# Performance work log

Hardware: AMD Instinct MI355X
Metric: run time of the kernel (lower is better)

The kernel has to match this reference:

```python
import jax, jax.numpy as jnp
import numpy as np

DIM = 1024
HEADS = 16
DIM_HEAD = 64
INNER = HEADS * DIM_HEAD
EPS = 1e-5


def layernorm(x, g, b):
    mu = jnp.mean(x, axis=-1, keepdims=True)
    var = jnp.mean((x - mu) ** 2, axis=-1, keepdims=True)
    return (x - mu) * jax.lax.rsqrt(var + EPS) * g + b


def setup_inputs() -> dict:
    key = jax.random.key(0)
    ks = jax.random.split(key, 8)
    B, S = 2, 2048
    s_in = (2.0 / DIM) ** 0.5
    return {
        "x": jax.random.normal(ks[0], (B, S, DIM), jnp.float32),
        "w_qkv": jax.random.normal(ks[1], (DIM, 3 * INNER), jnp.float32) * s_in,
        "w_out": jax.random.normal(ks[2], (INNER, DIM), jnp.float32) * s_in,
        "b_out": jnp.zeros((DIM,), jnp.float32),
        "g1": jnp.ones((DIM,), jnp.float32),
        "beta1": jnp.zeros((DIM,), jnp.float32),
        "g2": jnp.ones((DIM,), jnp.float32),
        "beta2": jnp.zeros((DIM,), jnp.float32),
        "w_ff1": jax.random.normal(ks[3], (DIM, 4 * DIM), jnp.float32) * s_in,
        "b_ff1": jnp.zeros((4 * DIM,), jnp.float32),
        "w_ff2": jax.random.normal(ks[4], (4 * DIM, DIM), jnp.float32) * (2.0 / (4 * DIM)) ** 0.5,
        "b_ff2": jnp.zeros((DIM,), jnp.float32),
    }


def reference(x, w_qkv, w_out, b_out, g1, beta1, g2, beta2, w_ff1, b_ff1, w_ff2, b_ff2):
    B, S, D = x.shape
    scale = DIM_HEAD ** -0.5
    # --- attention block (pre-norm) ---
    h = layernorm(x, g1, beta1)
    qkv = h @ w_qkv  # [B,S,3*INNER]
    q, k, v = jnp.split(qkv, 3, axis=-1)
    def heads(t):
        return t.reshape(B, S, HEADS, DIM_HEAD).transpose(0, 2, 1, 3)  # [B,H,S,dh]
    q, k, v = heads(q), heads(k), heads(v)
    attn = jnp.einsum("bhsd,bhtd->bhst", q, k) * scale
    attn = jax.nn.softmax(attn, axis=-1)
    out = jnp.einsum("bhst,bhtd->bhsd", attn, v)
    out = out.transpose(0, 2, 1, 3).reshape(B, S, INNER)
    x = x + out @ w_out + b_out
    # --- FFN block (pre-norm) ---
    h = layernorm(x, g2, beta2)
    h = jax.nn.gelu(h @ w_ff1 + b_ff1, approximate=False)
    x = x + h @ w_ff2 + b_ff2
    return x
```

## Files before the change

### kernel.cpp

```cpp
#include <hip/hip_runtime.h>
#include <math.h>

typedef unsigned short u16;
typedef __attribute__((ext_vector_type(4))) float f32x4;
typedef __attribute__((ext_vector_type(16))) float f32x16;
typedef __attribute__((ext_vector_type(4))) unsigned short u16x4;
typedef __attribute__((ext_vector_type(8))) __bf16 bf16x8;

static constexpr int SS   = 2048;
static constexpr int DD   = 1024;
static constexpr int HH   = 16;
static constexpr int DH   = 64;
static constexpr int NTOK = 4096;
static constexpr int NQKV = 3072;

#define DEV static __device__ __forceinline__
#define GLD_AS1(p) ((__attribute__((address_space(1))) void*)(void*)(p))
#define GLD_AS3(p) ((__attribute__((address_space(3))) void*)(p))

#define WAIT_BAR(N) asm volatile("s_waitcnt vmcnt(" #N ")\n\ts_barrier" ::: "memory")
#define BAR()       asm volatile("s_barrier" ::: "memory")

DEV u16 f2bf(float f) {
    union { float f; unsigned int i; } v; v.f = f;
    unsigned int r = v.i + 0x7fffu + ((v.i >> 16) & 1u);
    return (u16)(r >> 16);
}
DEV float bdec(u16 u) {
    union { unsigned int i; float f; } v; v.i = ((unsigned int)u) << 16; return v.f;
}

DEV f32x4 MFMA(bf16x8 a, bf16x8 b, f32x4 c) {
    return __builtin_amdgcn_mfma_f32_16x16x32_bf16(a, b, c, 0, 0, 0);
}
DEV f32x16 MFMA32(bf16x8 a, bf16x8 b, f32x16 c) {
    return __builtin_amdgcn_mfma_f32_32x32x16_bf16(a, b, c, 0, 0, 0);
}
DEV f32x16 zero16() {
    f32x16 z;
    #pragma unroll
    for (int i = 0; i < 16; i++) z[i] = 0.f;
    return z;
}

__global__ __launch_bounds__(256)
void k_transpose(const float* __restrict__ in, u16* __restrict__ out, int R, int C) {
    __shared__ float tile[32][33];
    int c0 = blockIdx.x * 32, r0 = blockIdx.y * 32;
    int tx = threadIdx.x, ty = threadIdx.y;
    #pragma unroll
    for (int i = 0; i < 32; i += 8)
        tile[ty + i][tx] = in[(size_t)(r0 + ty + i) * C + c0 + tx];
    __syncthreads();
    #pragma unroll
    for (int i = 0; i < 32; i += 8)
        out[(size_t)(c0 + ty + i) * R + r0 + tx] = f2bf(tile[tx][ty + i]);
}

__global__ __launch_bounds__(256)
void k_transpose_v(const u16* __restrict__ qkv, u16* __restrict__ vT) {
    __shared__ u16 tile[32][33];
    int bid = blockIdx.x;
    int st = bid & 63;
    int dt = (bid >> 6) & 1;
    int bh = bid >> 7;
    int b = bh >> 4, h = bh & 15;
    int s0 = st * 32, d0 = dt * 32;
    int tx = threadIdx.x & 31, ty = threadIdx.x >> 5;
    const u16* src = qkv + ((size_t)(b * SS + s0)) * NQKV + 2048 + h * DH + d0;
    #pragma unroll
    for (int i = 0; i < 32; i += 8)
        tile[ty + i][tx] = src[(size_t)(ty + i) * NQKV + tx];
    __syncthreads();
    u16* dst = vT + ((size_t)bh * DH + d0) * SS + s0;
    #pragma unroll
    for (int i = 0; i < 32; i += 8)
        dst[(size_t)(ty + i) * SS + tx] = tile[tx][ty + i];
}

__global__ __launch_bounds__(256)
void k_layernorm(const float* __restrict__ x, const float* __restrict__ g,
                 const float* __restrict__ b, u16* __restrict__ out) {
    int row = blockIdx.x, t = threadIdx.x;
    const float4* xp = reinterpret_cast<const float4*>(x + (size_t)row * DD);
    float4 v = xp[t];
    float s = v.x + v.y + v.z + v.w;
    float q = v.x * v.x + v.y * v.y + v.z * v.z + v.w * v.w;
    #pragma unroll
    for (int m = 1; m < 64; m <<= 1) { s += __shfl_xor(s, m); q += __shfl_xor(q, m); }
    __shared__ float ps[4], pq[4];
    int w = t >> 6, l = t & 63;
    if (l == 0) { ps[w] = s; pq[w] = q; }
    __syncthreads();
    s = ps[0] + ps[1] + ps[2] + ps[3];
    q = pq[0] + pq[1] + pq[2] + pq[3];
    float mu = s * (1.0f / DD);
    float var = q * (1.0f / DD) - mu * mu;
    float rstd = rsqrtf(var + 1e-5f);
    float4 gv = reinterpret_cast<const float4*>(g)[t];
    float4 bv = reinterpret_cast<const float4*>(b)[t];
    u16x4 o;
    o.x = f2bf((v.x - mu) * rstd * gv.x + bv.x);
    o.y = f2bf((v.y - mu) * rstd * gv.y + bv.y);
    o.z = f2bf((v.z - mu) * rstd * gv.z + bv.z);
    o.w = f2bf((v.w - mu) * rstd * gv.w + bv.w);
    reinterpret_cast<u16x4*>(out + (size_t)row * DD)[t] = o;
}

__global__ __launch_bounds__(256)
void k_redln(const float* __restrict__ x, const u16* __restrict__ P0,
             const u16* __restrict__ P1, const float* __restrict__ bias,
             const float* __restrict__ g, const float* __restrict__ be,
             float* __restrict__ X1, u16* __restrict__ LNout) {
    int row = blockIdx.x, t = threadIdx.x;
    size_t i = (size_t)row * 256 + t;
    float4 xv = reinterpret_cast<const float4*>(x)[i];
    u16x4 a = reinterpret_cast<const u16x4*>(P0)[i];
    u16x4 bb = reinterpret_cast<const u16x4*>(P1)[i];
    float4 bv = reinterpret_cast<const float4*>(bias)[t];
    float4 v;
    v.x = xv.x + bdec(a.x) + bdec(bb.x) + bv.x;
    v.y = xv.y + bdec(a.y) + bdec(bb.y) + bv.y;
    v.z = xv.z + bdec(a.z) + bdec(bb.z) + bv.z;
    v.w = xv.w + bdec(a.w) + bdec(bb.w) + bv.w;
    reinterpret_cast<float4*>(X1)[i] = v;
    float s = v.x + v.y + v.z + v.w;
    float q = v.x * v.x + v.y * v.y + v.z * v.z + v.w * v.w;
    #pragma unroll
    for (int m = 1; m < 64; m <<= 1) { s += __shfl_xor(s, m); q += __shfl_xor(q, m); }
    __shared__ float ps[4], pq[4];
    int w = t >> 6, l = t & 63;
    if (l == 0) { ps[w] = s; pq[w] = q; }
    __syncthreads();
    s = ps[0] + ps[1] + ps[2] + ps[3];
    q = pq[0] + pq[1] + pq[2] + pq[3];
    float mu = s * (1.0f / DD);
    float var = q * (1.0f / DD) - mu * mu;
    float rstd = rsqrtf(var + 1e-5f);
    float4 gv = reinterpret_cast<const float4*>(g)[t];
    float4 ev = reinterpret_cast<const float4*>(be)[t];
    u16x4 o;
    o.x = f2bf((v.x - mu) * rstd * gv.x + ev.x);
    o.y = f2bf((v.y - mu) * rstd * gv.y + ev.y);
    o.z = f2bf((v.z - mu) * rstd * gv.z + ev.z);
    o.w = f2bf((v.w - mu) * rstd * gv.w + ev.w);
    reinterpret_cast<u16x4*>(LNout + (size_t)row * DD)[t] = o;
}

template<int MODE>
__global__ __launch_bounds__(256)
void k_gemm(const u16* __restrict__ A, const u16* __restrict__ BT,
            float* __restrict__ Cf, u16* __restrict__ Cb,
            const float* __restrict__ bias, const float* __restrict__ res,
            u16* __restrict__ vT, int M, int N, int K) {
    __shared__ __align__(128) char lds[2][32768];
    const int t = threadIdx.x;
    const int w = t >> 6, l = t & 63;
    const int lg = l >> 4, lr = l & 15;
    const int m0 = blockIdx.y * 128, n0 = blockIdx.x * 128;
    const int wr = w >> 1, wc = w & 1;

    int kbeg = 0, kend = K;
    if (MODE == 3) {
        const int kh = K >> 1;
        kbeg = blockIdx.z * kh;
        kend = kbeg + kh;
    }

    const int csw = ((l & 7) ^ (l >> 3)) << 3;
    const int chunk0 = w * 4;
    const int srow = (l >> 3);

    f32x4 acc[4][4];
    #pragma unroll
    for (int i = 0; i < 4; i++)
        #pragma unroll
        for (int j = 0; j < 4; j++)
            acc[i][j] = (f32x4){0.f, 0.f, 0.f, 0.f};

    #pragma unroll
    for (int i = 0; i < 4; i++) {
        const int chunk = chunk0 + i;
        const int r = chunk * 8 + srow;
        __builtin_amdgcn_global_load_lds(GLD_AS1(A  + (size_t)(m0 + r) * K + kbeg + csw),
                                         GLD_AS3(lds[0] + chunk * 1024), 16, 0, 0);
        __builtin_amdgcn_global_load_lds(GLD_AS1(BT + (size_t)(n0 + r) * K + kbeg + csw),
                                         GLD_AS3(lds[0] + 16384 + chunk * 1024), 16, 0, 0);
    }

    int buf = 0;
    for (int kt = kbeg; kt < kend; kt += 64) {
        if (kt + 64 < kend) {
            #pragma unroll
            for (int i = 0; i < 4; i++) {
                const int chunk = chunk0 + i;
                const int r = chunk * 8 + srow;
                __builtin_amdgcn_global_load_lds(GLD_AS1(A  + (size_t)(m0 + r) * K + kt + 64 + csw),
                                                 GLD_AS3(lds[buf ^ 1] + chunk * 1024), 16, 0, 0);
                __builtin_amdgcn_global_load_lds(GLD_AS1(BT + (size_t)(n0 + r) * K + kt + 64 + csw),
                                                 GLD_AS3(lds[buf ^ 1] + 16384 + chunk * 1024), 16, 0, 0);
            }
            WAIT_BAR(8);
        } else {
            WAIT_BAR(0);
        }
        const char* Al = lds[buf];
        const char* Bl = lds[buf] + 16384;
        #pragma unroll
        for (int s = 0; s < 2; s++) {
            const int swz = (s * 64 + lg * 16) ^ ((lr & 7) << 4);
            bf16x8 af[4], bfr[4];
            #pragma unroll
            for (int mi = 0; mi < 4; mi++)
                af[mi] = *reinterpret_cast<const bf16x8*>(Al + (wr * 64 + mi * 16 + lr) * 128 + swz);
            #pragma unroll
            for (int ni = 0; ni < 4; ni++)
                bfr[ni] = *reinterpret_cast<const bf16x8*>(Bl + (wc * 64 + ni * 16 + lr) * 128 + swz);
            #pragma unroll
            for (int mi = 0; mi < 4; mi++)
                #pragma unroll
                for (int ni = 0; ni < 4; ni++)
                    acc[mi][ni] = MFMA(af[mi], bfr[ni], acc[mi][ni]);
        }
        BAR();
        buf ^= 1;
    }

    #pragma unroll
    for (int mi = 0; mi < 4; mi++) {
        #pragma unroll
        for (int ni = 0; ni < 4; ni++) {
            int nn = n0 + wc * 64 + ni * 16 + lr;
            #pragma unroll
            for (int r = 0; r < 4; r++) {
                int mm = m0 + wr * 64 + mi * 16 + lg * 4 + r;
                float v = acc[mi][ni][r];
                if (MODE == 0) {
                    float sv = (nn < 1024) ? v * 0.18033688011112042f : v;
                    Cb[(size_t)mm * NQKV + nn] = f2bf(sv);
                } else if (MODE == 2) {
                    float u = v + bias[nn];
                    float u3 = u * u * u;
                    float gl = u / (1.0f + exp2f(-2.3022077f * u - 0.10294276f * u3));
                    Cb[(size_t)mm * N + nn] = f2bf(gl);
                } else {
                    u16* dst = blockIdx.z ? vT : Cb;
                    dst[(size_t)mm * N + nn] = f2bf(v);
                }
            }
        }
    }
}

__global__ __launch_bounds__(256)
void k_ffreduce(const float* __restrict__ RES, const u16* __restrict__ P0,
                const u16* __restrict__ P1, const float* __restrict__ bias,
                float* __restrict__ OUT) {
    int i = blockIdx.x * 256 + threadIdx.x;
    float4 xv = reinterpret_cast<const float4*>(RES)[i];
    u16x4 a = reinterpret_cast<const u16x4*>(P0)[i];
    u16x4 b = reinterpret_cast<const u16x4*>(P1)[i];
    float4 bv = reinterpret_cast<const float4*>(bias)[i & (DD / 4 - 1)];
    float4 o;
    o.x = xv.x + bdec(a.x) + bdec(b.x) + bv.x;
    o.y = xv.y + bdec(a.y) + bdec(b.y) + bv.y;
    o.z = xv.z + bdec(a.z) + bdec(b.z) + bv.z;
    o.w = xv.w + bdec(a.w) + bdec(b.w) + bv.w;
    reinterpret_cast<float4*>(OUT)[i] = o;
}

__global__ __launch_bounds__(256)
void k_attn(const u16* __restrict__ qkv, const u16* __restrict__ vT,
            u16* __restrict__ out) {
    const int w = threadIdx.x >> 6, l = threadIdx.x & 63;
    const int q = l & 31, hi = l >> 5;
    const int task = (blockIdx.x & 7) * 64 + (blockIdx.x >> 3);
    const int bh = task >> 4;
    const int qg = task & 15;
    const int b = bh >> 4, h = bh & 15;
    const size_t rowbase = (size_t)b * SS;
    const int q0 = (qg * 4 + w) * 32;

    __shared__ __align__(128) u16 Kl[2][64 * 64];
    __shared__ __align__(128) u16 Vl[2][64 * 64];

    const u16* kbase = qkv + rowbase * NQKV + 1024 + h * DH;
    const u16* vbase = vT + (size_t)bh * DH * SS;

    const int srow8 = l >> 3;
    const int sslot = (l & 7) ^ srow8;
    const int kr0 = w * 8 + srow8;
    const u16* kg0 = kbase + (size_t)kr0 * NQKV + sslot * 8;
    const u16* kg1 = kbase + (size_t)(kr0 + 32) * NQKV + sslot * 8;
    const u16* vg0 = vbase + (size_t)kr0 * SS + sslot * 8;
    const u16* vg1 = vbase + (size_t)(kr0 + 32) * SS + sslot * 8;
    const int chA = (w * 8) * 64, chB = (w * 8 + 32) * 64;

    const u16* qrow = qkv + (rowbase + q0 + q) * NQKV + h * DH + hi * 8;
    bf16x8 qf[4];
    #pragma unroll
    for (int ks = 0; ks < 4; ks++)
        qf[ks] = *reinterpret_cast<const bf16x8*>(qrow + ks * 16);
    asm volatile("s_waitcnt vmcnt(0)" ::: "memory");

    bf16x8 onesf;
    #pragma unroll
    for (int i = 0; i < 8; i++) onesf[i] = (__bf16)1.0f;

    f32x16 o0 = zero16(), o1 = zero16();
    f32x16 lacc = zero16();

    __builtin_amdgcn_global_load_lds(GLD_AS1(kg0), GLD_AS3((u16*)Kl[0] + chA), 16, 0, 0);
    __builtin_amdgcn_global_load_lds(GLD_AS1(kg1), GLD_AS3((u16*)Kl[0] + chB), 16, 0, 0);
    __builtin_amdgcn_global_load_lds(GLD_AS1(vg0), GLD_AS3((u16*)Vl[0] + chA), 16, 0, 0);
    __builtin_amdgcn_global_load_lds(GLD_AS1(vg1), GLD_AS3((u16*)Vl[0] + chB), 16, 0, 0);

    int buf = 0;
    for (int kv0 = 0; kv0 < SS; kv0 += 64) {
        if (kv0 + 64 < SS) {
            __builtin_amdgcn_global_load_lds(GLD_AS1(kg0 + (size_t)(kv0 + 64) * NQKV),
                                             GLD_AS3((u16*)Kl[buf ^ 1] + chA), 16, 0, 0);
            __builtin_amdgcn_global_load_lds(GLD_AS1(kg1 + (size_t)(kv0 + 64) * NQKV),
                                             GLD_AS3((u16*)Kl[buf ^ 1] + chB), 16, 0, 0);
            __builtin_amdgcn_global_load_lds(GLD_AS1(vg0 + (kv0 + 64)),
                                             GLD_AS3((u16*)Vl[buf ^ 1] + chA), 16, 0, 0);
            __builtin_amdgcn_global_load_lds(GLD_AS1(vg1 + (kv0 + 64)),
                                             GLD_AS3((u16*)Vl[buf ^ 1] + chB), 16, 0, 0);
            WAIT_BAR(4);
        } else {
            WAIT_BAR(0);
        }
        const u16* Kb = Kl[buf];
        const u16* Vb = Vl[buf];
        const int qsw = (q & 7) << 3;

        f32x16 st0 = zero16(), st1 = zero16();
        #pragma unroll
        for (int ks = 0; ks < 4; ks++) {
            const int off = (ks * 16 + hi * 8) ^ qsw;
            bf16x8 kf0 = *reinterpret_cast<const bf16x8*>(Kb + q * 64 + off);
            bf16x8 kf1 = *reinterpret_cast<const bf16x8*>(Kb + (q + 32) * 64 + off);
            st0 = MFMA32(kf0, qf[ks], st0);
            st1 = MFMA32(kf1, qf[ks], st1);
        }

        f32x16 p0, p1;
        #pragma unroll
        for (int i = 0; i < 16; i++) p0[i] = exp2f(st0[i]);
        #pragma unroll
        for (int i = 0; i < 16; i++) p1[i] = exp2f(st1[i]);

        union W { unsigned int u; __bf16 h[2]; };
        W pw[16];
        #pragma unroll
        for (int m = 0; m < 8; m++) {
            pw[m].h[0] = (__bf16)p0[2 * m];
            pw[m].h[1] = (__bf16)p0[2 * m + 1];
            pw[8 + m].h[0] = (__bf16)p1[2 * m];
            pw[8 + m].h[1] = (__bf16)p1[2 * m + 1];
        }

        bf16x8 pf[4];
        #pragma unroll
        for (int kk = 0; kk < 4; kk++) {
            const int base = (kk >> 1) * 8 + (kk & 1) * 4;
            unsigned int a0 = pw[base + 0].u, a1 = pw[base + 1].u;
            unsigned int b0 = pw[base + 2].u, b1 = pw[base + 3].u;
            unsigned int own0 = hi ? b0 : a0, own1 = hi ? b1 : a1;
            unsigned int snd0 = hi ? a0 : b0, snd1 = hi ? a1 : b1;
            unsigned int r0 = __shfl_xor(snd0, 32), r1 = __shfl_xor(snd1, 32);
            union F { unsigned int u[4]; bf16x8 v; } f;
            f.u[0] = hi ? r0 : own0;
            f.u[1] = hi ? r1 : own1;
            f.u[2] = hi ? own0 : r0;
            f.u[3] = hi ? own1 : r1;
            pf[kk] = f.v;
        }

        #pragma unroll
        for (int kk = 0; kk < 4; kk++) {
            const int off = (kk * 16 + hi * 8) ^ qsw;
            bf16x8 v0 = *reinterpret_cast<const bf16x8*>(Vb + q * 64 + off);
            bf16x8 v1 = *reinterpret_cast<const bf16x8*>(Vb + (q + 32) * 64 + off);
            lacc = MFMA32(onesf, pf[kk], lacc);
            o0 = MFMA32(v0, pf[kk], o0);
            o1 = MFMA32(v1, pf[kk], o1);
        }

        BAR();
        buf ^= 1;
    }

    float invl = 1.0f / lacc[0];
    u16* orow = out + (rowbase + q0 + q) * DD + h * DH + hi * 4;
    #pragma unroll
    for (int a = 0; a < 4; a++) {
        u16x4 s0v, s1v;
        #pragma unroll
        for (int i = 0; i < 4; i++) {
            s0v[i] = f2bf(o0[4 * a + i] * invl);
            s1v[i] = f2bf(o1[4 * a + i] * invl);
        }
        *reinterpret_cast<u16x4*>(orow + 8 * a)      = s0v;
        *reinterpret_cast<u16x4*>(orow + 32 + 8 * a) = s1v;
    }
}

extern "C" void kernel_launch(void* const* d_in, const int* in_sizes, int n_in,
                              void* d_out, int out_size, void* d_ws, size_t ws_size,
                              hipStream_t stream) {
    (void)in_sizes; (void)n_in; (void)out_size; (void)ws_size;
    const float* x     = (const float*)d_in[0];
    const float* w_qkv = (const float*)d_in[1];
    const float* w_out = (const float*)d_in[2];
    const float* b_out = (const float*)d_in[3];
    const float* g1    = (const float*)d_in[4];
    const float* be1   = (const float*)d_in[5];
    const float* g2    = (const float*)d_in[6];
    const float* be2   = (const float*)d_in[7];
    const float* w_ff1 = (const float*)d_in[8];
    const float* b_ff1 = (const float*)d_in[9];
    const float* w_ff2 = (const float*)d_in[10];
    const float* b_ff2 = (const float*)d_in[11];

    char* ws = (char*)d_ws;
    u16*   W  = (u16*)(ws);
    u16*   Hb = (u16*)(ws + 8388608);
    u16*   QF = (u16*)(ws + 16777216);
    u16*   VT = (u16*)(ws + 50331648);
    u16*   AO = (u16*)(ws + 58720256);
    float* X1 = (float*)(ws + 67108864);
    float* OUT = (float*)d_out;

    k_layernorm<<<NTOK, 256, 0, stream>>>(x, g1, be1, Hb);
    k_transpose<<<dim3(3072 / 32, 1024 / 32), dim3(32, 8), 0, stream>>>(w_qkv, W, 1024, 3072);
    k_gemm<0><<<dim3(3072 / 128, 4096 / 128), 256, 0, stream>>>(
        Hb, W, nullptr, QF, nullptr, nullptr, nullptr, NTOK, NQKV, 1024);
    k_transpose_v<<<4096, 256, 0, stream>>>(QF, VT);
    k_attn<<<512, 256, 0, stream>>>(QF, VT, AO);
    k_transpose<<<dim3(1024 / 32, 1024 / 32), dim3(32, 8), 0, stream>>>(w_out, W, 1024, 1024);
    k_gemm<3><<<dim3(1024 / 128, 4096 / 128, 2), 256, 0, stream>>>(
        AO, W, nullptr, Hb, nullptr, nullptr, VT, NTOK, 1024, 1024);
    k_redln<<<NTOK, 256, 0, stream>>>(x, Hb, VT, b_out, g2, be2, X1, AO);
    k_transpose<<<dim3(4096 / 32, 1024 / 32), dim3(32, 8), 0, stream>>>(w_ff1, W, 1024, 4096);
    k_gemm<2><<<dim3(4096 / 128, 4096 / 128), 256, 0, stream>>>(
        AO, W, nullptr, QF, b_ff1, nullptr, nullptr, NTOK, 4096, 1024);
    k_transpose<<<dim3(1024 / 32, 4096 / 32), dim3(32, 8), 0, stream>>>(w_ff2, W, 4096, 1024);
    k_gemm<3><<<dim3(1024 / 128, 4096 / 128, 2), 256, 0, stream>>>(
        QF, W, nullptr, VT, nullptr, nullptr, Hb, NTOK, 1024, 4096);
    k_ffreduce<<<NTOK * DD / 4 / 256, 256, 0, stream>>>(X1, VT, Hb, b_ff2, OUT);
}
```

Before: 266.0 us.

## Software-pipeline attention loop so next QK^T overlaps current softmax and PV

The attention main loop is restructured so the QK^T scores for the next KV tile are computed while the exponentials and PV products of the current tile are processed. K gets a three-stage LDS ring and V keeps a separate double buffer, with V loads issued one iteration later than K. The trailing barrier of each iteration is removed, leaving one wait-and-barrier per iteration. The aim is to hide the exp and MFMA latency chain and reduce synchronisation, at the cost of more LDS and registers for a second set of score accumulators.

```diff
diff --git a/kernel.cpp b/kernel.cpp
--- a/kernel.cpp
+++ b/kernel.cpp
@@ -19,7 +19,6 @@
 #define GLD_AS3(p) ((__attribute__((address_space(3))) void*)(p))
 
 #define WAIT_BAR(N) asm volatile("s_waitcnt vmcnt(" #N ")\n\ts_barrier" ::: "memory")
-#define BAR()       asm volatile("s_barrier" ::: "memory")
 
 DEV u16 f2bf(float f) {
     union { float f; unsigned int i; } v; v.f = f;
@@ -222,7 +221,7 @@
                 for (int ni = 0; ni < 4; ni++)
                     acc[mi][ni] = MFMA(af[mi], bfr[ni], acc[mi][ni]);
         }
-        BAR();
+        asm volatile("s_barrier" ::: "memory");
         buf ^= 1;
     }
 
@@ -281,7 +280,7 @@
     const size_t rowbase = (size_t)b * SS;
     const int q0 = (qg * 4 + w) * 32;
 
-    __shared__ __align__(128) u16 Kl[2][64 * 64];
+    __shared__ __align__(128) u16 Kl[3][64 * 64];
     __shared__ __align__(128) u16 Vl[2][64 * 64];
 
     const u16* kbase = qkv + rowbase * NQKV + 1024 + h * DH;
@@ -309,46 +308,64 @@
 
     f32x16 o0 = zero16(), o1 = zero16();
     f32x16 lacc = zero16();
+    const int qsw = (q & 7) << 3;
 
     __builtin_amdgcn_global_load_lds(GLD_AS1(kg0), GLD_AS3((u16*)Kl[0] + chA), 16, 0, 0);
     __builtin_amdgcn_global_load_lds(GLD_AS1(kg1), GLD_AS3((u16*)Kl[0] + chB), 16, 0, 0);
+    __builtin_amdgcn_global_load_lds(GLD_AS1(kg0 + (size_t)64 * NQKV), GLD_AS3((u16*)Kl[1] + chA), 16, 0, 0);
+    __builtin_amdgcn_global_load_lds(GLD_AS1(kg1 + (size_t)64 * NQKV), GLD_AS3((u16*)Kl[1] + chB), 16, 0, 0);
     __builtin_amdgcn_global_load_lds(GLD_AS1(vg0), GLD_AS3((u16*)Vl[0] + chA), 16, 0, 0);
     __builtin_amdgcn_global_load_lds(GLD_AS1(vg1), GLD_AS3((u16*)Vl[0] + chB), 16, 0, 0);
-
-    int buf = 0;
-    for (int kv0 = 0; kv0 < SS; kv0 += 64) {
-        if (kv0 + 64 < SS) {
-            __builtin_amdgcn_global_load_lds(GLD_AS1(kg0 + (size_t)(kv0 + 64) * NQKV),
-                                             GLD_AS3((u16*)Kl[buf ^ 1] + chA), 16, 0, 0);
-            __builtin_amdgcn_global_load_lds(GLD_AS1(kg1 + (size_t)(kv0 + 64) * NQKV),
-                                             GLD_AS3((u16*)Kl[buf ^ 1] + chB), 16, 0, 0);
-            __builtin_amdgcn_global_load_lds(GLD_AS1(vg0 + (kv0 + 64)),
-                                             GLD_AS3((u16*)Vl[buf ^ 1] + chA), 16, 0, 0);
-            __builtin_amdgcn_global_load_lds(GLD_AS1(vg1 + (kv0 + 64)),
-                                             GLD_AS3((u16*)Vl[buf ^ 1] + chB), 16, 0, 0);
-            WAIT_BAR(4);
-        } else {
-            WAIT_BAR(0);
-        }
-        const u16* Kb = Kl[buf];
-        const u16* Vb = Vl[buf];
-        const int qsw = (q & 7) << 3;
-
-        f32x16 st0 = zero16(), st1 = zero16();
+    WAIT_BAR(4);
+
+    f32x16 scA0 = zero16(), scA1 = zero16();
+    {
+        const u16* Kb = Kl[0];
         #pragma unroll
         for (int ks = 0; ks < 4; ks++) {
             const int off = (ks * 16 + hi * 8) ^ qsw;
             bf16x8 kf0 = *reinterpret_cast<const bf16x8*>(Kb + q * 64 + off);
             bf16x8 kf1 = *reinterpret_cast<const bf16x8*>(Kb + (q + 32) * 64 + off);
-            st0 = MFMA32(kf0, qf[ks], st0);
-            st1 = MFMA32(kf1, qf[ks], st1);
+            scA0 = MFMA32(kf0, qf[ks], scA0);
+            scA1 = MFMA32(kf1, qf[ks], scA1);
+        }
+    }
+
+    int kRead = 1, vRead = 0;
+    for (int i = 0; i < 32; ++i) {
+        const int kStage = (kRead == 2) ? 0 : kRead + 1;
+        if (i + 2 < 32) {
+            const size_t koff = (size_t)(i + 2) * 64 * NQKV;
+            __builtin_amdgcn_global_load_lds(GLD_AS1(kg0 + koff), GLD_AS3((u16*)Kl[kStage] + chA), 16, 0, 0);
+            __builtin_amdgcn_global_load_lds(GLD_AS1(kg1 + koff), GLD_AS3((u16*)Kl[kStage] + chB), 16, 0, 0);
+            WAIT_BAR(2);
+        } else {
+            WAIT_BAR(0);
+        }
+        if (i + 1 < 32) {
+            const int voff = (i + 1) * 64;
+            __builtin_amdgcn_global_load_lds(GLD_AS1(vg0 + voff), GLD_AS3((u16*)Vl[vRead ^ 1] + chA), 16, 0, 0);
+            __builtin_amdgcn_global_load_lds(GLD_AS1(vg1 + voff), GLD_AS3((u16*)Vl[vRead ^ 1] + chB), 16, 0, 0);
         }
 
         f32x16 p0, p1;
         #pragma unroll
-        for (int i = 0; i < 16; i++) p0[i] = exp2f(st0[i]);
-        #pragma unroll
-        for (int i = 0; i < 16; i++) p1[i] = exp2f(st1[i]);
+        for (int j = 0; j < 16; j++) p0[j] = exp2f(scA0[j]);
+        #pragma unroll
+        for (int j = 0; j < 16; j++) p1[j] = exp2f(scA1[j]);
+
+        f32x16 stB0 = zero16(), stB1 = zero16();
+        if (i + 1 < 32) {
+            const u16* Kb = Kl[kRead];
+            #pragma unroll
+            for (int ks = 0; ks < 4; ks++) {
+                const int off = (ks * 16 + hi * 8) ^ qsw;
+                bf16x8 kf0 = *reinterpret_cast<const bf16x8*>(Kb + q * 64 + off);
+                bf16x8 kf1 = *reinterpret_cast<const bf16x8*>(Kb + (q + 32) * 64 + off);
+                stB0 = MFMA32(kf0, qf[ks], stB0);
+                stB1 = MFMA32(kf1, qf[ks], stB1);
+            }
+        }
 
         union W { unsigned int u; __bf16 h[2]; };
         W pw[16];
@@ -359,7 +376,6 @@
             pw[8 + m].h[0] = (__bf16)p1[2 * m];
             pw[8 + m].h[1] = (__bf16)p1[2 * m + 1];
         }
-
         bf16x8 pf[4];
         #pragma unroll
         for (int kk = 0; kk < 4; kk++) {
@@ -377,6 +393,7 @@
             pf[kk] = f.v;
         }
 
+        const u16* Vb = Vl[vRead];
         #pragma unroll
         for (int kk = 0; kk < 4; kk++) {
             const int off = (kk * 16 + hi * 8) ^ qsw;
@@ -387,8 +404,10 @@
             o1 = MFMA32(v1, pf[kk], o1);
         }
 
-        BAR();
-        buf ^= 1;
+        scA0 = stB0;
+        scA1 = stB1;
+        kRead = kStage;
+        vRead ^= 1;
     }
 
     float invl = 1.0f / lacc[0];
```

Result: faster. 255.6 us (-3.9%).
